# Performance work log

Hardware: AMD Instinct MI355X
Metric: run time of the kernel (lower is better)

The kernel has to match this reference:

```python
import jax, jax.numpy as jnp
import numpy as np

B, C, H, W = 128, 3, 256, 256


def setup_inputs() -> dict:
    key = jax.random.key(0)
    k1, k2, k3, k4 = jax.random.split(key, 4)
    img = jax.random.uniform(k1, (B, C, H, W), jnp.float32)
    # init in the module: rot=PI, trans=0, scale=1, shear=0; add small noise
    rot = jnp.pi + 0.5 * jax.random.normal(k2, (B, 1), jnp.float32)
    trans = 0.1 * jax.random.normal(k3, (B, 2), jnp.float32)
    scale = jnp.ones((B, 1), jnp.float32)
    shear = 0.1 * jax.random.normal(k4, (B, 2), jnp.float32)
    return {"img": img, "rot": rot, "trans": trans, "scale": scale, "shear": shear}


def _theta(rot, trans, scale, shear):
    # 2x3 affine matrix per sample: A = scale * R(rot) @ Shear, last col = trans
    r = rot[:, 0]
    s = scale[:, 0]
    c, sn = jnp.cos(r), jnp.sin(r)
    shx, shy = shear[:, 0], shear[:, 1]
    a00 = s * (c - sn * shy)
    a01 = s * (c * shx - sn)
    a10 = s * (sn + c * shy)
    a11 = s * (sn * shx + c)
    row0 = jnp.stack([a00, a01, trans[:, 0]], axis=-1)  # [B,3]
    row1 = jnp.stack([a10, a11, trans[:, 1]], axis=-1)  # [B,3]
    return jnp.stack([row0, row1], axis=1)  # [B,2,3]


def _affine_grid(theta, Hc, Wc):
    # normalized coords, align_corners=False convention
    ys = (2.0 * (jnp.arange(Hc, dtype=jnp.float32) + 0.5) / Hc) - 1.0
    xs = (2.0 * (jnp.arange(Wc, dtype=jnp.float32) + 0.5) / Wc) - 1.0
    gx, gy = jnp.meshgrid(xs, ys)  # [H,W]
    base = jnp.stack([gx, gy, jnp.ones_like(gx)], axis=-1)  # [H,W,3]
    return jnp.einsum('bij,hwj->bhwi', theta, base)  # [B,H,W,2] -> (x,y)


def _grid_sample(img, grid):
    # bilinear, zeros padding, align_corners=False
    Bc, Cc, Hc, Wc = img.shape
    ix = ((grid[..., 0] + 1.0) * Wc - 1.0) / 2.0
    iy = ((grid[..., 1] + 1.0) * Hc - 1.0) / 2.0
    x0 = jnp.floor(ix); y0 = jnp.floor(iy)
    x1 = x0 + 1.0; y1 = y0 + 1.0
    wx1 = ix - x0; wx0 = 1.0 - wx1
    wy1 = iy - y0; wy0 = 1.0 - wy1
    flat = img.reshape(Bc, Cc, Hc * Wc)

    def gather(xi, yi, w):
        valid = (xi >= 0) & (xi <= Wc - 1) & (yi >= 0) & (yi <= Hc - 1)
        xc = jnp.clip(xi, 0, Wc - 1).astype(jnp.int32)
        yc = jnp.clip(yi, 0, Hc - 1).astype(jnp.int32)
        idx = (yc * Wc + xc).reshape(Bc, 1, -1)  # [B,1,H*W]
        vals = jnp.take_along_axis(flat, idx, axis=2)  # [B,C,H*W]
        wm = (w * valid.astype(w.dtype)).reshape(Bc, 1, -1)
        return vals * wm

    out = (gather(x0, y0, wx0 * wy0) + gather(x1, y0, wx1 * wy0)
           + gather(x0, y1, wx0 * wy1) + gather(x1, y1, wx1 * wy1))
    return out.reshape(Bc, Cc, Hc, Wc)


def reference(img, rot, trans, scale, shear):
    theta = _theta(rot, trans, scale, shear)
    grid = _affine_grid(theta, img.shape[2], img.shape[3])
    return _grid_sample(img, grid)
```

## Files before the change

kernel.cpp:

```cpp
#include <hip/hip_runtime.h>
#include <math.h>

#define BATCH 128
#define CHAN  3
#define IMH   256
#define IMW   256
#define NXCD  8
#define TW    32
#define TH    16

#define BH_T   42
#define BW_T   45
#define NC_MAX 44

__global__ __launch_bounds__(256) void affine_sample_kernel(
        const float* __restrict__ img,
        const float* __restrict__ rot,
        const float* __restrict__ trans,
        const float* __restrict__ scale,
        const float* __restrict__ shear,
        float* __restrict__ out) {
    __shared__ float tile[CHAN][BH_T][BW_T];

    const int NBLK = BATCH * (IMH / TH) * (IMW / TW);
    const int p = blockIdx.x;
    const int L = (p & (NXCD - 1)) * (NBLK / NXCD) + (p >> 3);

    const int b  = L >> 7;
    const int tl = L & 127;
    const int w0 = (tl & 7) * TW;
    const int h0 = (tl >> 3) * TH;

    const float r   = rot[b];
    const float s   = scale[b];
    const float shx = shear[2 * b + 0];
    const float shy = shear[2 * b + 1];
    const float txr = trans[2 * b + 0];
    const float tyr = trans[2 * b + 1];
    const float c  = __cosf(r);
    const float sn = __sinf(r);
    const float a00 = s * (c - sn * shy);
    const float a01 = s * (c * shx - sn);
    const float a10 = s * (sn + c * shy);
    const float a11 = s * (sn * shx + c);
    const float g0x = 1.0f / (float)IMW - 1.0f;
    const float g0y = 1.0f / (float)IMH - 1.0f;
    const float Cx = ((a00 * g0x + a01 * g0y + txr + 1.0f) * (float)IMW - 1.0f) * 0.5f;
    const float Cy = ((a10 * g0x + a11 * g0y + tyr + 1.0f) * (float)IMH - 1.0f) * 0.5f;
    const float hx = 15.5f * fabsf(a00) + 7.5f * fabsf(a01);
    const float hy = 15.5f * fabsf(a10) + 7.5f * fabsf(a11);

    const float ixc = Cx + a00 * ((float)w0 + 15.5f) + a01 * ((float)h0 + 7.5f);
    const float iyc = Cy + a10 * ((float)w0 + 15.5f) + a11 * ((float)h0 + 7.5f);
    const int xlu = (int)floorf(ixc - hx);
    const int xhu = (int)floorf(ixc + hx) + 1;
    const int ylu = (int)floorf(iyc - hy);
    const int yhu = (int)floorf(iyc + hy) + 1;
    const bool interior = (xlu >= 1) & (xhu <= IMW - 2) & (ylu >= 1) & (yhu <= IMH - 2);

    const int x_lo = min(max(xlu, 0), IMW - 1);
    const int x_hi = min(max(xhu, 0), IMW - 1);
    const int y_lo = min(max(ylu, 0), IMH - 1);
    const int y_hi = min(max(yhu, 0), IMH - 1);
    const int xs  = (x_lo - 1) & ~1;
    const int ys  = y_lo - 1;
    const int ncs = x_hi + 2 - xs;
    const int nrs = y_hi + 2 - ys;

    const int t  = threadIdx.x;
    const int wq = w0 + (t & 31);
    const int hq = h0 + ((t >> 5) << 1);
    const float ixa = Cx + a00 * (float)wq + a01 * (float)hq;
    const float iya = Cy + a10 * (float)wq + a11 * (float)hq;
    const float ixb = ixa + a01;
    const float iyb = iya + a11;

    const float x0fa = floorf(ixa), y0fa = floorf(iya);
    const float x0fb = floorf(ixb), y0fb = floorf(iyb);
    const float wx1a = ixa - x0fa, wy1a = iya - y0fa;
    const float wx1b = ixb - x0fb, wy1b = iyb - y0fb;
    const float wx0a = 1.0f - wx1a, wy0a = 1.0f - wy1a;
    const float wx0b = 1.0f - wx1b, wy0b = 1.0f - wy1b;

    float w00a, w10a, w01a, w11a, w00b, w10b, w01b, w11b;
    if (interior) {
        w00a = wx0a * wy0a; w10a = wx1a * wy0a;
        w01a = wx0a * wy1a; w11a = wx1a * wy1a;
        w00b = wx0b * wy0b; w10b = wx1b * wy0b;
        w01b = wx0b * wy1b; w11b = wx1b * wy1b;
    } else {
        const bool vx0a = (x0fa >= 0.0f) & (x0fa <= (float)(IMW - 1));
        const bool vx1a = (x0fa >= -1.0f) & (x0fa <= (float)(IMW - 2));
        const bool vy0a = (y0fa >= 0.0f) & (y0fa <= (float)(IMH - 1));
        const bool vy1a = (y0fa >= -1.0f) & (y0fa <= (float)(IMH - 2));
        w00a = (vx0a && vy0a) ? (wx0a * wy0a) : 0.0f;
        w10a = (vx1a && vy0a) ? (wx1a * wy0a) : 0.0f;
        w01a = (vx0a && vy1a) ? (wx0a * wy1a) : 0.0f;
        w11a = (vx1a && vy1a) ? (wx1a * wy1a) : 0.0f;
        const bool vx0b = (x0fb >= 0.0f) & (x0fb <= (float)(IMW - 1));
        const bool vx1b = (x0fb >= -1.0f) & (x0fb <= (float)(IMW - 2));
        const bool vy0b = (y0fb >= 0.0f) & (y0fb <= (float)(IMH - 1));
        const bool vy1b = (y0fb >= -1.0f) & (y0fb <= (float)(IMH - 2));
        w00b = (vx0b && vy0b) ? (wx0b * wy0b) : 0.0f;
        w10b = (vx1b && vy0b) ? (wx1b * wy0b) : 0.0f;
        w01b = (vx0b && vy1b) ? (wx0b * wy1b) : 0.0f;
        w11b = (vx1b && vy1b) ? (wx1b * wy1b) : 0.0f;
    }

    const int x0ia = (int)x0fa, y0ia = (int)y0fa;
    const int x0ib = (int)x0fb, y0ib = (int)y0fb;

    const int plane = IMH * IMW;
    const int obase = (b * CHAN) * plane + hq * IMW + wq;
    const float* ibase = img + (size_t)(b * CHAN) * plane;

    if (ncs <= NC_MAX && nrs <= BH_T) {
        const int lx2 = (t & 31) << 1;
        const int lyr = t >> 5;
        const int nrd = (nrs + 7) >> 3;
        const bool wcol = lx2 < ncs;
        const int xg = min(max(xs + lx2, 0), IMW - 2);
        for (int rr = 0; rr < nrd; ++rr) {
            const int dy = (rr << 3) + lyr;
            if (wcol & (dy < nrs)) {
                const int yg = min(max(ys + dy, 0), IMH - 1);
                const float* src = ibase + yg * IMW + xg;
                const float2 v0 = *(const float2*)(src);
                const float2 v1 = *(const float2*)(src + plane);
                const float2 v2 = *(const float2*)(src + 2 * plane);
                tile[0][dy][lx2]     = v0.x;
                tile[0][dy][lx2 + 1] = v0.y;
                tile[1][dy][lx2]     = v1.x;
                tile[1][dy][lx2 + 1] = v1.y;
                tile[2][dy][lx2]     = v2.x;
                tile[2][dy][lx2 + 1] = v2.y;
            }
        }
        __syncthreads();

        int rxa, rya, rxb, ryb;
        if (interior) {
            rxa = x0ia - xs;  rya = y0ia - ys;
            rxb = x0ib - xs;  ryb = y0ib - ys;
        } else {
            rxa = min(max(x0ia - xs, 0), ncs - 2);
            rya = min(max(y0ia - ys, 0), nrs - 2);
            rxb = min(max(x0ib - xs, 0), ncs - 2);
            ryb = min(max(y0ib - ys, 0), nrs - 2);
        }
#pragma unroll
        for (int cc = 0; cc < CHAN; ++cc) {
            const float* tpa = &tile[cc][rya][rxa];
            const float* tpb = &tile[cc][ryb][rxb];
            const float va = w00a * tpa[0] + w10a * tpa[1]
                           + w01a * tpa[BW_T] + w11a * tpa[BW_T + 1];
            const float vb = w00b * tpb[0] + w10b * tpb[1]
                           + w01b * tpb[BW_T] + w11b * tpb[BW_T + 1];
            out[obase + cc * plane]       = va;
            out[obase + cc * plane + IMW] = vb;
        }
    } else {
        const int x0ca = min(max(x0ia, 0), IMW - 1);
        const int x1ca = min(max(x0ia + 1, 0), IMW - 1);
        const int y0ca = min(max(y0ia, 0), IMH - 1);
        const int y1ca = min(max(y0ia + 1, 0), IMH - 1);
        const int x0cb = min(max(x0ib, 0), IMW - 1);
        const int x1cb = min(max(x0ib + 1, 0), IMW - 1);
        const int y0cb = min(max(y0ib, 0), IMH - 1);
        const int y1cb = min(max(y0ib + 1, 0), IMH - 1);
#pragma unroll
        for (int cc = 0; cc < CHAN; ++cc) {
            const float* p2 = ibase + cc * plane;
            const float va = w00a * p2[y0ca * IMW + x0ca] + w10a * p2[y0ca * IMW + x1ca]
                           + w01a * p2[y1ca * IMW + x0ca] + w11a * p2[y1ca * IMW + x1ca];
            const float vb = w00b * p2[y0cb * IMW + x0cb] + w10b * p2[y0cb * IMW + x1cb]
                           + w01b * p2[y1cb * IMW + x0cb] + w11b * p2[y1cb * IMW + x1cb];
            out[obase + cc * plane]       = va;
            out[obase + cc * plane + IMW] = vb;
        }
    }
}

extern "C" void kernel_launch(void* const* d_in, const int* in_sizes, int n_in,
                              void* d_out, int out_size, void* d_ws, size_t ws_size,
                              hipStream_t stream) {
    const float* img   = (const float*)d_in[0];
    const float* rot   = (const float*)d_in[1];
    const float* trans = (const float*)d_in[2];
    const float* scale = (const float*)d_in[3];
    const float* shear = (const float*)d_in[4];
    float* out = (float*)d_out;

    const int nblocks = BATCH * (IMH / TH) * (IMW / TW);
    affine_sample_kernel<<<nblocks, 256, 0, stream>>>(img, rot, trans, scale,
                                                      shear, out);
}
```

Baseline: 41.72 us.

## Interleave channels in shared tile and process two row-halves per block

Changes the shared-memory tile from channel-planar to channel-interleaved rows (stride 132), so the three channel reads for a sample hit adjacent addresses. Each block now covers a 32x32 output tile in two sequential 32x16 halves, reusing the shared buffer with an extra barrier. This halves the block count and amortizes per-block affine setup, but serializes the two halves inside a block and lowers the number of concurrent blocks.

Result: slower. 43.37 us (+4.0%).

```diff
diff --git a/kernel.cpp b/kernel.cpp
--- a/kernel.cpp
+++ b/kernel.cpp
@@ -10,8 +10,8 @@
 #define TH    16
 
 #define BH_T   42
-#define BW_T   45
 #define NC_MAX 44
+#define ROWSTR 132
 
 __global__ __launch_bounds__(256) void affine_sample_kernel(
         const float* __restrict__ img,
@@ -20,16 +20,16 @@
         const float* __restrict__ scale,
         const float* __restrict__ shear,
         float* __restrict__ out) {
-    __shared__ float tile[CHAN][BH_T][BW_T];
-
-    const int NBLK = BATCH * (IMH / TH) * (IMW / TW);
+    __shared__ float tile[BH_T * ROWSTR];
+
+    const int NBLK = BATCH * 64;
     const int p = blockIdx.x;
     const int L = (p & (NXCD - 1)) * (NBLK / NXCD) + (p >> 3);
 
-    const int b  = L >> 7;
-    const int tl = L & 127;
+    const int b  = L >> 6;
+    const int tl = L & 63;
     const int w0 = (tl & 7) * TW;
-    const int h0 = (tl >> 3) * TH;
+    const int h0 = (tl >> 3) * (2 * TH);
 
     const float r   = rot[b];
     const float s   = scale[b];
@@ -50,133 +50,141 @@
     const float hx = 15.5f * fabsf(a00) + 7.5f * fabsf(a01);
     const float hy = 15.5f * fabsf(a10) + 7.5f * fabsf(a11);
 
-    const float ixc = Cx + a00 * ((float)w0 + 15.5f) + a01 * ((float)h0 + 7.5f);
-    const float iyc = Cy + a10 * ((float)w0 + 15.5f) + a11 * ((float)h0 + 7.5f);
-    const int xlu = (int)floorf(ixc - hx);
-    const int xhu = (int)floorf(ixc + hx) + 1;
-    const int ylu = (int)floorf(iyc - hy);
-    const int yhu = (int)floorf(iyc + hy) + 1;
-    const bool interior = (xlu >= 1) & (xhu <= IMW - 2) & (ylu >= 1) & (yhu <= IMH - 2);
-
-    const int x_lo = min(max(xlu, 0), IMW - 1);
-    const int x_hi = min(max(xhu, 0), IMW - 1);
-    const int y_lo = min(max(ylu, 0), IMH - 1);
-    const int y_hi = min(max(yhu, 0), IMH - 1);
-    const int xs  = (x_lo - 1) & ~1;
-    const int ys  = y_lo - 1;
-    const int ncs = x_hi + 2 - xs;
-    const int nrs = y_hi + 2 - ys;
-
     const int t  = threadIdx.x;
     const int wq = w0 + (t & 31);
-    const int hq = h0 + ((t >> 5) << 1);
-    const float ixa = Cx + a00 * (float)wq + a01 * (float)hq;
-    const float iya = Cy + a10 * (float)wq + a11 * (float)hq;
-    const float ixb = ixa + a01;
-    const float iyb = iya + a11;
-
-    const float x0fa = floorf(ixa), y0fa = floorf(iya);
-    const float x0fb = floorf(ixb), y0fb = floorf(iyb);
-    const float wx1a = ixa - x0fa, wy1a = iya - y0fa;
-    const float wx1b = ixb - x0fb, wy1b = iyb - y0fb;
-    const float wx0a = 1.0f - wx1a, wy0a = 1.0f - wy1a;
-    const float wx0b = 1.0f - wx1b, wy0b = 1.0f - wy1b;
-
-    float w00a, w10a, w01a, w11a, w00b, w10b, w01b, w11b;
-    if (interior) {
-        w00a = wx0a * wy0a; w10a = wx1a * wy0a;
-        w01a = wx0a * wy1a; w11a = wx1a * wy1a;
-        w00b = wx0b * wy0b; w10b = wx1b * wy0b;
-        w01b = wx0b * wy1b; w11b = wx1b * wy1b;
-    } else {
-        const bool vx0a = (x0fa >= 0.0f) & (x0fa <= (float)(IMW - 1));
-        const bool vx1a = (x0fa >= -1.0f) & (x0fa <= (float)(IMW - 2));
-        const bool vy0a = (y0fa >= 0.0f) & (y0fa <= (float)(IMH - 1));
-        const bool vy1a = (y0fa >= -1.0f) & (y0fa <= (float)(IMH - 2));
-        w00a = (vx0a && vy0a) ? (wx0a * wy0a) : 0.0f;
-        w10a = (vx1a && vy0a) ? (wx1a * wy0a) : 0.0f;
-        w01a = (vx0a && vy1a) ? (wx0a * wy1a) : 0.0f;
-        w11a = (vx1a && vy1a) ? (wx1a * wy1a) : 0.0f;
-        const bool vx0b = (x0fb >= 0.0f) & (x0fb <= (float)(IMW - 1));
-        const bool vx1b = (x0fb >= -1.0f) & (x0fb <= (float)(IMW - 2));
-        const bool vy0b = (y0fb >= 0.0f) & (y0fb <= (float)(IMH - 1));
-        const bool vy1b = (y0fb >= -1.0f) & (y0fb <= (float)(IMH - 2));
-        w00b = (vx0b && vy0b) ? (wx0b * wy0b) : 0.0f;
-        w10b = (vx1b && vy0b) ? (wx1b * wy0b) : 0.0f;
-        w01b = (vx0b && vy1b) ? (wx0b * wy1b) : 0.0f;
-        w11b = (vx1b && vy1b) ? (wx1b * wy1b) : 0.0f;
-    }
-
-    const int x0ia = (int)x0fa, y0ia = (int)y0fa;
-    const int x0ib = (int)x0fb, y0ib = (int)y0fb;
-
+    const int hoff = (t >> 5) << 1;
+    const int lx2 = (t & 31) << 1;
+    const int lyr = t >> 5;
     const int plane = IMH * IMW;
-    const int obase = (b * CHAN) * plane + hq * IMW + wq;
     const float* ibase = img + (size_t)(b * CHAN) * plane;
 
-    if (ncs <= NC_MAX && nrs <= BH_T) {
-        const int lx2 = (t & 31) << 1;
-        const int lyr = t >> 5;
-        const int nrd = (nrs + 7) >> 3;
-        const bool wcol = lx2 < ncs;
-        const int xg = min(max(xs + lx2, 0), IMW - 2);
-        for (int rr = 0; rr < nrd; ++rr) {
-            const int dy = (rr << 3) + lyr;
-            if (wcol & (dy < nrs)) {
-                const int yg = min(max(ys + dy, 0), IMH - 1);
-                const float* src = ibase + yg * IMW + xg;
-                const float2 v0 = *(const float2*)(src);
-                const float2 v1 = *(const float2*)(src + plane);
-                const float2 v2 = *(const float2*)(src + 2 * plane);
-                tile[0][dy][lx2]     = v0.x;
-                tile[0][dy][lx2 + 1] = v0.y;
-                tile[1][dy][lx2]     = v1.x;
-                tile[1][dy][lx2 + 1] = v1.y;
-                tile[2][dy][lx2]     = v2.x;
-                tile[2][dy][lx2 + 1] = v2.y;
+    for (int half = 0; half < 2; ++half) {
+        const int h0h = h0 + half * TH;
+
+        const float ixc = Cx + a00 * ((float)w0 + 15.5f) + a01 * ((float)h0h + 7.5f);
+        const float iyc = Cy + a10 * ((float)w0 + 15.5f) + a11 * ((float)h0h + 7.5f);
+        const int xlu = (int)floorf(ixc - hx);
+        const int xhu = (int)floorf(ixc + hx) + 1;
+        const int ylu = (int)floorf(iyc - hy);
+        const int yhu = (int)floorf(iyc + hy) + 1;
+        const bool interior = (xlu >= 1) & (xhu <= IMW - 2) &
+                              (ylu >= 1) & (yhu <= IMH - 2);
+
+        const int x_lo = min(max(xlu, 0), IMW - 1);
+        const int x_hi = min(max(xhu, 0), IMW - 1);
+        const int y_lo = min(max(ylu, 0), IMH - 1);
+        const int y_hi = min(max(yhu, 0), IMH - 1);
+        const int xs  = (x_lo - 1) & ~1;
+        const int ys  = y_lo - 1;
+        const int ncs = x_hi + 2 - xs;
+        const int nrs = y_hi + 2 - ys;
+        const bool fits = (ncs <= NC_MAX) & (nrs <= BH_T);
+
+        const int hq = h0h + hoff;
+        const float ixa = Cx + a00 * (float)wq + a01 * (float)hq;
+        const float iya = Cy + a10 * (float)wq + a11 * (float)hq;
+        const float ixb = ixa + a01;
+        const float iyb = iya + a11;
+
+        const float x0fa = floorf(ixa), y0fa = floorf(iya);
+        const float x0fb = floorf(ixb), y0fb = floorf(iyb);
+        const float wx1a = ixa - x0fa, wy1a = iya - y0fa;
+        const float wx1b = ixb - x0fb, wy1b = iyb - y0fb;
+        const float wx0a = 1.0f - wx1a, wy0a = 1.0f - wy1a;
+        const float wx0b = 1.0f - wx1b, wy0b = 1.0f - wy1b;
+
+        float w00a, w10a, w01a, w11a, w00b, w10b, w01b, w11b;
+        if (interior) {
+            w00a = wx0a * wy0a; w10a = wx1a * wy0a;
+            w01a = wx0a * wy1a; w11a = wx1a * wy1a;
+            w00b = wx0b * wy0b; w10b = wx1b * wy0b;
+            w01b = wx0b * wy1b; w11b = wx1b * wy1b;
+        } else {
+            const bool vx0a = (x0fa >= 0.0f) & (x0fa <= (float)(IMW - 1));
+            const bool vx1a = (x0fa >= -1.0f) & (x0fa <= (float)(IMW - 2));
+            const bool vy0a = (y0fa >= 0.0f) & (y0fa <= (float)(IMH - 1));
+            const bool vy1a = (y0fa >= -1.0f) & (y0fa <= (float)(IMH - 2));
+            w00a = (vx0a && vy0a) ? (wx0a * wy0a) : 0.0f;
+            w10a = (vx1a && vy0a) ? (wx1a * wy0a) : 0.0f;
+            w01a = (vx0a && vy1a) ? (wx0a * wy1a) : 0.0f;
+            w11a = (vx1a && vy1a) ? (wx1a * wy1a) : 0.0f;
+            const bool vx0b = (x0fb >= 0.0f) & (x0fb <= (float)(IMW - 1));
+            const bool vx1b = (x0fb >= -1.0f) & (x0fb <= (float)(IMW - 2));
+            const bool vy0b = (y0fb >= 0.0f) & (y0fb <= (float)(IMH - 1));
+            const bool vy1b = (y0fb >= -1.0f) & (y0fb <= (float)(IMH - 2));
+            w00b = (vx0b && vy0b) ? (wx0b * wy0b) : 0.0f;
+            w10b = (vx1b && vy0b) ? (wx1b * wy0b) : 0.0f;
+            w01b = (vx0b && vy1b) ? (wx0b * wy1b) : 0.0f;
+            w11b = (vx1b && vy1b) ? (wx1b * wy1b) : 0.0f;
+        }
+
+        const int x0ia = (int)x0fa, y0ia = (int)y0fa;
+        const int x0ib = (int)x0fb, y0ib = (int)y0fb;
+        const int obase = (b * CHAN) * plane + hq * IMW + wq;
+
+        if (half) __syncthreads();
+
+        if (fits) {
+            const int nrd = (nrs + 7) >> 3;
+            const bool wcol = lx2 < ncs;
+            const int xg = min(max(xs + lx2, 0), IMW - 2);
+            for (int rr = 0; rr < nrd; ++rr) {
+                const int dy = (rr << 3) + lyr;
+                if (wcol & (dy < nrs)) {
+                    const int yg = min(max(ys + dy, 0), IMH - 1);
+                    const float* src = ibase + yg * IMW + xg;
+                    const float2 v0 = *(const float2*)(src);
+                    const float2 v1 = *(const float2*)(src + plane);
+                    const float2 v2 = *(const float2*)(src + 2 * plane);
+                    float* dst = &tile[dy * ROWSTR + lx2 * 3];
+                    dst[0] = v0.x; dst[1] = v1.x; dst[2] = v2.x;
+                    dst[3] = v0.y; dst[4] = v1.y; dst[5] = v2.y;
+                }
             }
         }
         __syncthreads();
 
-        int rxa, rya, rxb, ryb;
-        if (interior) {
-            rxa = x0ia - xs;  rya = y0ia - ys;
-            rxb = x0ib - xs;  ryb = y0ib - ys;
+        if (fits) {
+            int rxa, rya, rxb, ryb;
+            if (interior) {
+                rxa = x0ia - xs;  rya = y0ia - ys;
+                rxb = x0ib - xs;  ryb = y0ib - ys;
+            } else {
+                rxa = min(max(x0ia - xs, 0), ncs - 2);
+                rya = min(max(y0ia - ys, 0), nrs - 2);
+                rxb = min(max(x0ib - xs, 0), ncs - 2);
+                ryb = min(max(y0ib - ys, 0), nrs - 2);
+            }
+            const float* tpa = &tile[rya * ROWSTR + rxa * 3];
+            const float* tpb = &tile[ryb * ROWSTR + rxb * 3];
+#pragma unroll
+            for (int cc = 0; cc < CHAN; ++cc) {
+                const float va = w00a * tpa[cc]          + w10a * tpa[cc + 3]
+                               + w01a * tpa[cc + ROWSTR] + w11a * tpa[cc + ROWSTR + 3];
+                const float vb = w00b * tpb[cc]          + w10b * tpb[cc + 3]
+                               + w01b * tpb[cc + ROWSTR] + w11b * tpb[cc + ROWSTR + 3];
+                out[obase + cc * plane]       = va;
+                out[obase + cc * plane + IMW] = vb;
+            }
         } else {
-            rxa = min(max(x0ia - xs, 0), ncs - 2);
-            rya = min(max(y0ia - ys, 0), nrs - 2);
-            rxb = min(max(x0ib - xs, 0), ncs - 2);
-            ryb = min(max(y0ib - ys, 0), nrs - 2);
-        }
+            const int x0ca = min(max(x0ia, 0), IMW - 1);
+            const int x1ca = min(max(x0ia + 1, 0), IMW - 1);
+            const int y0ca = min(max(y0ia, 0), IMH - 1);
+            const int y1ca = min(max(y0ia + 1, 0), IMH - 1);
+            const int x0cb = min(max(x0ib, 0), IMW - 1);
+            const int x1cb = min(max(x0ib + 1, 0), IMW - 1);
+            const int y0cb = min(max(y0ib, 0), IMH - 1);
+            const int y1cb = min(max(y0ib + 1, 0), IMH - 1);
 #pragma unroll
-        for (int cc = 0; cc < CHAN; ++cc) {
-            const float* tpa = &tile[cc][rya][rxa];
-            const float* tpb = &tile[cc][ryb][rxb];
-            const float va = w00a * tpa[0] + w10a * tpa[1]
-                           + w01a * tpa[BW_T] + w11a * tpa[BW_T + 1];
-            const float vb = w00b * tpb[0] + w10b * tpb[1]
-                           + w01b * tpb[BW_T] + w11b * tpb[BW_T + 1];
-            out[obase + cc * plane]       = va;
-            out[obase + cc * plane + IMW] = vb;
-        }
-    } else {
-        const int x0ca = min(max(x0ia, 0), IMW - 1);
-        const int x1ca = min(max(x0ia + 1, 0), IMW - 1);
-        const int y0ca = min(max(y0ia, 0), IMH - 1);
-        const int y1ca = min(max(y0ia + 1, 0), IMH - 1);
-        const int x0cb = min(max(x0ib, 0), IMW - 1);
-        const int x1cb = min(max(x0ib + 1, 0), IMW - 1);
-        const int y0cb = min(max(y0ib, 0), IMH - 1);
-        const int y1cb = min(max(y0ib + 1, 0), IMH - 1);
-#pragma unroll
-        for (int cc = 0; cc < CHAN; ++cc) {
-            const float* p2 = ibase + cc * plane;
-            const float va = w00a * p2[y0ca * IMW + x0ca] + w10a * p2[y0ca * IMW + x1ca]
-                           + w01a * p2[y1ca * IMW + x0ca] + w11a * p2[y1ca * IMW + x1ca];
-            const float vb = w00b * p2[y0cb * IMW + x0cb] + w10b * p2[y0cb * IMW + x1cb]
-                           + w01b * p2[y1cb * IMW + x0cb] + w11b * p2[y1cb * IMW + x1cb];
-            out[obase + cc * plane]       = va;
-            out[obase + cc * plane + IMW] = vb;
+            for (int cc = 0; cc < CHAN; ++cc) {
+                const float* p2 = ibase + cc * plane;
+                const float va = w00a * p2[y0ca * IMW + x0ca] + w10a * p2[y0ca * IMW + x1ca]
+                               + w01a * p2[y1ca * IMW + x0ca] + w11a * p2[y1ca * IMW + x1ca];
+                const float vb = w00b * p2[y0cb * IMW + x0cb] + w10b * p2[y0cb * IMW + x1cb]
+                               + w01b * p2[y1cb * IMW + x0cb] + w11b * p2[y1cb * IMW + x1cb];
+                out[obase + cc * plane]       = va;
+                out[obase + cc * plane + IMW] = vb;
+            }
         }
     }
 }
@@ -191,7 +199,7 @@
     const float* shear = (const float*)d_in[4];
     float* out = (float*)d_out;
 
-    const int nblocks = BATCH * (IMH / TH) * (IMW / TW);
+    const int nblocks = BATCH * 64;
     affine_sample_kernel<<<nblocks, 256, 0, stream>>>(img, rot, trans, scale,
                                                       shear, out);
 }
```
